# Performance work log

Hardware: AMD Instinct MI355X
Metric: run time of the kernel (lower is better)

The kernel has to match this reference:

```python
import jax, jax.numpy as jnp
import numpy as np

N_NODES = 100000
N_EDGES = 1250000
D = 64
K = 5
EPS = 1e-8


def setup_inputs() -> dict:
    key = jax.random.key(0)
    k1, k2, k3, k4 = jax.random.split(key, 4)
    x = jax.random.normal(k1, (N_NODES, D), dtype=jnp.float32)
    mask = jax.random.normal(k2, (N_NODES, 1), dtype=jnp.float32)
    edge_index = jax.random.randint(k3, (2, N_EDGES), 0, N_NODES, dtype=jnp.int64)
    # orthogonal-ish init for the linear layer (QR of gaussian), gain for tanh = 5/3
    g = jax.random.normal(k4, (D, D), dtype=jnp.float32)
    q, _ = jnp.linalg.qr(g)
    W = (5.0 / 3.0) * q.astype(jnp.float32)
    b = jnp.zeros((D,), dtype=jnp.float32)
    alpha = jnp.float32(0.001)
    return {"x": x, "mask": mask, "edge_index": edge_index, "W": W, "b": b, "alpha": alpha}


def _forward(x, mask, edge_index, W, b, alpha):
    n = x.shape[0]
    # x_fn: Linear + Tanh
    h = jnp.tanh(x @ W.T + b)  # [N, D]
    src = edge_index[0]
    dst = edge_index[1]
    hs = h[src]  # [E, D] gather
    hd = h[dst]  # [E, D] gather
    # torch cosine_similarity with eps clamp on each norm
    ns = jnp.maximum(jnp.sqrt(jnp.sum(hs * hs, axis=-1)), EPS)
    nd = jnp.maximum(jnp.sqrt(jnp.sum(hd * hd, axis=-1)), EPS)
    cos = jnp.sum(hs * hd, axis=-1) / (ns * nd)
    edge_weights = jax.nn.relu(cos)  # [E]

    # gcn_norm with self loops (PyG APPNP default): D^-1/2 (A + I) D^-1/2
    loop = jnp.arange(n, dtype=src.dtype)
    row = jnp.concatenate([src, loop])
    col = jnp.concatenate([dst, loop])
    w = jnp.concatenate([edge_weights, jnp.ones((n,), dtype=edge_weights.dtype)])
    deg = jax.ops.segment_sum(w, col, num_segments=n)
    dis = jnp.where(deg > 0, jax.lax.rsqrt(jnp.maximum(deg, EPS)), 0.0)
    norm_w = dis[row] * w * dis[col]  # [E + N]

    # APPNP: K steps of f = (1-alpha) * A_hat @ f + alpha * f0
    f0 = jax.nn.relu(mask)  # [N, 1]
    f = f0
    for _ in range(K):
        msg = norm_w[:, None] * f[row]  # gather + weight
        agg = jax.ops.segment_sum(msg, col, num_segments=n)  # scatter-add
        f = (1.0 - alpha) * agg + alpha * f0
    return f, edge_weights


def reference(x, mask, edge_index, W, b, alpha):
    return _forward(x, mask, edge_index, W, b, alpha)
```

## Files before the change

### kernel.cpp

```cpp
#include <hip/hip_runtime.h>
#include <hip/hip_fp16.h>
#include <math.h>

#define N_NODES 100000
#define N_EDGES 1250000
#define D 64
#define EPS 1e-8f

#define ZERO_BLOCKS 391
#define GEMM_BLOCKS 1024
#define RANK_BLOCKS 4883

__global__ __launch_bounds__(256) void k_gemm_zero(
    const float* __restrict__ x, const float* __restrict__ W,
    const float* __restrict__ b, __half* __restrict__ hn, int* __restrict__ cnt)
{
    if (blockIdx.x < ZERO_BLOCKS) {
        int i = blockIdx.x * 256 + threadIdx.x;
        if (i < N_NODES) cnt[i] = 0;
        return;
    }
    __shared__ float xrow[4][72];
    const int lane = threadIdx.x & 63;
    const int wid  = threadIdx.x >> 6;

    float Wreg[64];
    const float4* Wv = (const float4*)(W + lane * D);
    #pragma unroll
    for (int q = 0; q < 16; ++q) {
        float4 w4 = Wv[q];
        Wreg[4*q+0] = w4.x; Wreg[4*q+1] = w4.y;
        Wreg[4*q+2] = w4.z; Wreg[4*q+3] = w4.w;
    }
    const float bj = b[lane];
    float* xl = xrow[wid];

    const int wave   = (blockIdx.x - ZERO_BLOCKS) * 4 + wid;
    const int nwaves = GEMM_BLOCKS * 4;

    for (int row = wave; row < N_NODES; row += nwaves) {
        float xv = x[(size_t)row * D + lane];
        xl[lane] = xv;
        float acc = bj;
        #pragma unroll
        for (int q = 0; q < 16; ++q) {
            float4 xk4 = *(const float4*)(xl + 4*q);
            acc = fmaf(xk4.x, Wreg[4*q+0], acc);
            acc = fmaf(xk4.y, Wreg[4*q+1], acc);
            acc = fmaf(xk4.z, Wreg[4*q+2], acc);
            acc = fmaf(xk4.w, Wreg[4*q+3], acc);
        }
        float h = tanhf(acc);
        float s = h * h;
        #pragma unroll
        for (int m = 32; m >= 1; m >>= 1) s += __shfl_xor(s, m, 64);
        float nrm = fmaxf(sqrtf(s), EPS);
        hn[(size_t)row * D + lane] = __float2half_rn(h / nrm);
    }
}

__device__ __forceinline__ float dot8h(float4 a, float4 c)
{
    const __half2* ah = (const __half2*)&a;
    const __half2* ch = (const __half2*)&c;
    float p = 0.0f;
    #pragma unroll
    for (int q = 0; q < 4; ++q) {
        float2 af = __half22float2(ah[q]);
        float2 cf = __half22float2(ch[q]);
        p = fmaf(af.x, cf.x, p);
        p = fmaf(af.y, cf.y, p);
    }
    return p;
}

__global__ __launch_bounds__(256) void k_rank_cos(
    const int* __restrict__ ei, int* __restrict__ cnt, int* __restrict__ rank,
    const __half* __restrict__ hn, float* __restrict__ wout)
{
    const int b = blockIdx.x;
    const int r = b % 3;
    if (r == 0) {
        int e = (b / 3) * 256 + threadIdx.x;
        if (e < N_EDGES) {
            int d = ei[N_EDGES + e];
            rank[e] = atomicAdd(cnt + d, 1);
        }
        return;
    }
    int cb = (b / 3) * 2 + (r - 1);
    int t = cb * 256 + threadIdx.x;
    int g = t >> 3, sub = t & 7;
    if (g >= N_EDGES / 4) return;
    int e0 = g * 4;
    int4 ss = *(const int4*)(ei + e0);
    int4 dd = *(const int4*)(ei + N_EDGES + e0);

    float4 a0 = ((const float4*)(hn + (size_t)ss.x * D))[sub];
    float4 c0 = ((const float4*)(hn + (size_t)dd.x * D))[sub];
    float4 a1 = ((const float4*)(hn + (size_t)ss.y * D))[sub];
    float4 c1 = ((const float4*)(hn + (size_t)dd.y * D))[sub];
    float4 a2 = ((const float4*)(hn + (size_t)ss.z * D))[sub];
    float4 c2 = ((const float4*)(hn + (size_t)dd.z * D))[sub];
    float4 a3 = ((const float4*)(hn + (size_t)ss.w * D))[sub];
    float4 c3 = ((const float4*)(hn + (size_t)dd.w * D))[sub];

    float p0 = dot8h(a0, c0);
    float p1 = dot8h(a1, c1);
    float p2 = dot8h(a2, c2);
    float p3 = dot8h(a3, c3);
    p0 += __shfl_xor(p0, 1, 64);  p1 += __shfl_xor(p1, 1, 64);
    p2 += __shfl_xor(p2, 1, 64);  p3 += __shfl_xor(p3, 1, 64);
    p0 += __shfl_xor(p0, 2, 64);  p1 += __shfl_xor(p1, 2, 64);
    p2 += __shfl_xor(p2, 2, 64);  p3 += __shfl_xor(p3, 2, 64);
    p0 += __shfl_xor(p0, 4, 64);  p1 += __shfl_xor(p1, 4, 64);
    p2 += __shfl_xor(p2, 4, 64);  p3 += __shfl_xor(p3, 4, 64);

    if (sub == 0) {
        *(float4*)(wout + e0) = make_float4(
            fmaxf(p0, 0.0f), fmaxf(p1, 0.0f), fmaxf(p2, 0.0f), fmaxf(p3, 0.0f));
    }
}

__device__ __forceinline__ int wave_iscan(int v, int lane)
{
    int incl = v;
    #pragma unroll
    for (int m = 1; m < 64; m <<= 1) {
        int o = __shfl_up(incl, m, 64);
        if (lane >= m) incl += o;
    }
    return incl;
}

__global__ __launch_bounds__(256) void k_scan1(
    const int* __restrict__ cnt, int* __restrict__ rowptr, int* __restrict__ bsum)
{
    __shared__ int wsum[4];
    int t = threadIdx.x, b = blockIdx.x;
    int i = b * 256 + t;
    int lane = t & 63, wid = t >> 6;
    int v = (i < N_NODES) ? cnt[i] : 0;
    int incl = wave_iscan(v, lane);
    if (lane == 63) wsum[wid] = incl;
    __syncthreads();
    int off = 0;
    #pragma unroll
    for (int k = 0; k < 4; ++k) if (k < wid) off += wsum[k];
    if (i < N_NODES) rowptr[i] = off + incl - v;
    if (t == 255) bsum[b] = off + incl;
}

__global__ __launch_bounds__(512) void k_scan2(
    const int* __restrict__ bsum, int* __restrict__ boff, int nblk)
{
    __shared__ int wsum[8];
    int t = threadIdx.x;
    int lane = t & 63, wid = t >> 6;
    int v = (t < nblk) ? bsum[t] : 0;
    int incl = wave_iscan(v, lane);
    if (lane == 63) wsum[wid] = incl;
    __syncthreads();
    int off = 0;
    #pragma unroll
    for (int k = 0; k < 8; ++k) if (k < wid) off += wsum[k];
    if (t < nblk) boff[t] = off + incl - v;
}

__global__ __launch_bounds__(256) void k_scan3(
    int* __restrict__ rowptr, const int* __restrict__ boff)
{
    int i = blockIdx.x * 256 + threadIdx.x;
    if (i < N_NODES) rowptr[i] += boff[i >> 8];
    if (i == 0) rowptr[N_NODES] = N_EDGES;
}

__global__ __launch_bounds__(256) void k_place(
    const int* __restrict__ ei, const int* __restrict__ rank_pos,
    const int* __restrict__ rowptr, const float* __restrict__ wsrc,
    int2* __restrict__ pairs)
{
    int e = blockIdx.x * 256 + threadIdx.x;
    if (e >= N_EDGES) return;
    int s = ei[e];
    int d = ei[N_EDGES + e];
    int pos = rowptr[d] + rank_pos[e];
    pairs[pos] = make_int2(s, __float_as_int(wsrc[e]));
}

__global__ __launch_bounds__(256) void k_dis_y(
    const int* __restrict__ rowptr, const int2* __restrict__ pairs,
    const float* __restrict__ mask, float* __restrict__ dis,
    float* __restrict__ y)
{
    int t = blockIdx.x * 256 + threadIdx.x;
    int node = t >> 4, l = t & 15;
    if (node >= N_NODES) return;
    int beg = rowptr[node], end = rowptr[node + 1];
    float s = 0.0f;
    for (int j = beg + l; j < end; j += 16)
        s += __int_as_float(pairs[j].y);
    s += __shfl_xor(s, 1, 64);
    s += __shfl_xor(s, 2, 64);
    s += __shfl_xor(s, 4, 64);
    s += __shfl_xor(s, 8, 64);
    if (l == 0) {
        float di = rsqrtf(fmaxf(s + 1.0f, EPS));
        dis[node] = di;
        y[node] = di * fmaxf(mask[node], 0.0f);
    }
}

__global__ __launch_bounds__(256) void k_spmv(
    const int* __restrict__ rowptr, const int2* __restrict__ pairs,
    const float* __restrict__ y_in, const float* __restrict__ dis,
    const float* __restrict__ mask, const float* __restrict__ alpha_p,
    float* __restrict__ y_out, float* __restrict__ f_out)
{
    int t = blockIdx.x * 256 + threadIdx.x;
    int node = t >> 4, l = t & 15;
    if (node >= N_NODES) return;
    int beg = rowptr[node], end = rowptr[node + 1];
    float sum = 0.0f;
    for (int j = beg + l; j < end; j += 16) {
        int2 p = pairs[j];
        sum += __int_as_float(p.y) * y_in[p.x];
    }
    sum += __shfl_xor(sum, 1, 64);
    sum += __shfl_xor(sum, 2, 64);
    sum += __shfl_xor(sum, 4, 64);
    sum += __shfl_xor(sum, 8, 64);
    if (l == 0) {
        float di = dis[node];
        float alpha = alpha_p[0];
        float f0 = fmaxf(mask[node], 0.0f);
        float fn = (1.0f - alpha) * di * (sum + y_in[node]) + alpha * f0;
        f_out[node] = fn;
        y_out[node] = di * fn;
    }
}

extern "C" void kernel_launch(void* const* d_in, const int* in_sizes, int n_in,
                              void* d_out, int out_size, void* d_ws, size_t ws_size,
                              hipStream_t stream)
{
    const float* x     = (const float*)d_in[0];
    const float* mask  = (const float*)d_in[1];
    const int*   ei    = (const int*)  d_in[2];
    const float* W     = (const float*)d_in[3];
    const float* b     = (const float*)d_in[4];
    const float* alpha = (const float*)d_in[5];

    float* out_f = (float*)d_out;
    float* out_w = (float*)d_out + N_NODES;

    float* ws = (float*)d_ws;
    __half* hn     = (__half*)ws;
    int2*  pairs   = (int2*) (ws + 3200000);
    int*   rank    = (int*)  (ws + 5700000);
    int*   cnt     = (int*)  (ws + 6950000);
    int*   rowptr  = (int*)  (ws + 7050000);
    float* dis     =          ws + 7150016;
    float* y_a     =          ws + 7250016;
    float* y_b     =          ws + 7350016;
    float* f_scr   =          ws + 7450016;
    int*   bsum    = (int*)  (ws + 7550016);
    int*   boff    = (int*)  (ws + 7550528);

    const int nodeBlocks = (N_NODES + 255) / 256;
    const int edgeBlocks = (N_EDGES + 255) / 256;
    const int segBlocks  = (int)(((long long)N_NODES * 16 + 255) / 256);

    k_gemm_zero<<<ZERO_BLOCKS + GEMM_BLOCKS, 256, 0, stream>>>(x, W, b, hn, cnt);
    k_rank_cos<<<3 * RANK_BLOCKS, 256, 0, stream>>>(ei, cnt, rank, hn, out_w);
    k_scan1<<<nodeBlocks, 256, 0, stream>>>(cnt, rowptr, bsum);
    k_scan2<<<1, 512, 0, stream>>>(bsum, boff, nodeBlocks);
    k_scan3<<<nodeBlocks, 256, 0, stream>>>(rowptr, boff);
    k_place<<<edgeBlocks, 256, 0, stream>>>(ei, rank, rowptr, out_w, pairs);
    k_dis_y<<<segBlocks, 256, 0, stream>>>(rowptr, pairs, mask, dis, y_a);

    k_spmv<<<segBlocks, 256, 0, stream>>>(rowptr, pairs, y_a, dis, mask, alpha, y_b, f_scr);
    k_spmv<<<segBlocks, 256, 0, stream>>>(rowptr, pairs, y_b, dis, mask, alpha, y_a, f_scr);
    k_spmv<<<segBlocks, 256, 0, stream>>>(rowptr, pairs, y_a, dis, mask, alpha, y_b, f_scr);
    k_spmv<<<segBlocks, 256, 0, stream>>>(rowptr, pairs, y_b, dis, mask, alpha, y_a, f_scr);
    k_spmv<<<segBlocks, 256, 0, stream>>>(rowptr, pairs, y_a, dis, mask, alpha, y_b, out_f);
}
```

Baseline: 247.0 us.

## Fuse degree computation into cosine kernel, fold scan offsets, narrow SpMV lanes

```diff
diff --git a/kernel.cpp b/kernel.cpp
--- a/kernel.cpp
+++ b/kernel.cpp
@@ -10,14 +10,17 @@
 #define ZERO_BLOCKS 391
 #define GEMM_BLOCKS 1024
 #define RANK_BLOCKS 4883
+#define EDGE_BLOCKS 4883
+#define NODE_BLOCKS 391
 
 __global__ __launch_bounds__(256) void k_gemm_zero(
     const float* __restrict__ x, const float* __restrict__ W,
-    const float* __restrict__ b, __half* __restrict__ hn, int* __restrict__ cnt)
+    const float* __restrict__ b, __half* __restrict__ hn,
+    int* __restrict__ cnt, float* __restrict__ deg)
 {
     if (blockIdx.x < ZERO_BLOCKS) {
         int i = blockIdx.x * 256 + threadIdx.x;
-        if (i < N_NODES) cnt[i] = 0;
+        if (i < N_NODES) { cnt[i] = 0; deg[i] = 0.0f; }
         return;
     }
     __shared__ float xrow[4][72];
@@ -76,7 +79,8 @@
 
 __global__ __launch_bounds__(256) void k_rank_cos(
     const int* __restrict__ ei, int* __restrict__ cnt, int* __restrict__ rank,
-    const __half* __restrict__ hn, float* __restrict__ wout)
+    const __half* __restrict__ hn, float* __restrict__ wout,
+    float* __restrict__ deg)
 {
     const int b = blockIdx.x;
     const int r = b % 3;
@@ -117,8 +121,15 @@
     p2 += __shfl_xor(p2, 4, 64);  p3 += __shfl_xor(p3, 4, 64);
 
     if (sub == 0) {
-        *(float4*)(wout + e0) = make_float4(
-            fmaxf(p0, 0.0f), fmaxf(p1, 0.0f), fmaxf(p2, 0.0f), fmaxf(p3, 0.0f));
+        float w0 = fmaxf(p0, 0.0f);
+        float w1 = fmaxf(p1, 0.0f);
+        float w2 = fmaxf(p2, 0.0f);
+        float w3 = fmaxf(p3, 0.0f);
+        *(float4*)(wout + e0) = make_float4(w0, w1, w2, w3);
+        atomicAdd(deg + dd.x, w0);
+        atomicAdd(deg + dd.y, w1);
+        atomicAdd(deg + dd.z, w2);
+        atomicAdd(deg + dd.w, w3);
     }
 }
 
@@ -152,7 +163,8 @@
 }
 
 __global__ __launch_bounds__(512) void k_scan2(
-    const int* __restrict__ bsum, int* __restrict__ boff, int nblk)
+    const int* __restrict__ bsum, int* __restrict__ boff, int nblk,
+    int* __restrict__ rowptr)
 {
     __shared__ int wsum[8];
     int t = threadIdx.x;
@@ -165,71 +177,54 @@
     #pragma unroll
     for (int k = 0; k < 8; ++k) if (k < wid) off += wsum[k];
     if (t < nblk) boff[t] = off + incl - v;
-}
-
-__global__ __launch_bounds__(256) void k_scan3(
-    int* __restrict__ rowptr, const int* __restrict__ boff)
-{
-    int i = blockIdx.x * 256 + threadIdx.x;
-    if (i < N_NODES) rowptr[i] += boff[i >> 8];
-    if (i == 0) rowptr[N_NODES] = N_EDGES;
-}
-
-__global__ __launch_bounds__(256) void k_place(
+    if (t == 0) rowptr[N_NODES] = N_EDGES;
+}
+
+__global__ __launch_bounds__(256) void k_place_dis(
     const int* __restrict__ ei, const int* __restrict__ rank_pos,
-    const int* __restrict__ rowptr, const float* __restrict__ wsrc,
-    int2* __restrict__ pairs)
-{
+    const int* __restrict__ rowptr, const int* __restrict__ boff,
+    const float* __restrict__ wsrc, int2* __restrict__ pairs,
+    const float* __restrict__ deg, const float* __restrict__ mask,
+    float* __restrict__ dis, float* __restrict__ y)
+{
+    if (blockIdx.x >= EDGE_BLOCKS) {
+        int node = (blockIdx.x - EDGE_BLOCKS) * 256 + threadIdx.x;
+        if (node < N_NODES) {
+            float di = rsqrtf(fmaxf(deg[node] + 1.0f, EPS));
+            dis[node] = di;
+            y[node] = di * fmaxf(mask[node], 0.0f);
+        }
+        return;
+    }
     int e = blockIdx.x * 256 + threadIdx.x;
     if (e >= N_EDGES) return;
     int s = ei[e];
     int d = ei[N_EDGES + e];
-    int pos = rowptr[d] + rank_pos[e];
+    int pos = rowptr[d] + boff[d >> 8] + rank_pos[e];
     pairs[pos] = make_int2(s, __float_as_int(wsrc[e]));
 }
 
-__global__ __launch_bounds__(256) void k_dis_y(
-    const int* __restrict__ rowptr, const int2* __restrict__ pairs,
-    const float* __restrict__ mask, float* __restrict__ dis,
-    float* __restrict__ y)
-{
-    int t = blockIdx.x * 256 + threadIdx.x;
-    int node = t >> 4, l = t & 15;
-    if (node >= N_NODES) return;
-    int beg = rowptr[node], end = rowptr[node + 1];
-    float s = 0.0f;
-    for (int j = beg + l; j < end; j += 16)
-        s += __int_as_float(pairs[j].y);
-    s += __shfl_xor(s, 1, 64);
-    s += __shfl_xor(s, 2, 64);
-    s += __shfl_xor(s, 4, 64);
-    s += __shfl_xor(s, 8, 64);
-    if (l == 0) {
-        float di = rsqrtf(fmaxf(s + 1.0f, EPS));
-        dis[node] = di;
-        y[node] = di * fmaxf(mask[node], 0.0f);
-    }
-}
-
 __global__ __launch_bounds__(256) void k_spmv(
-    const int* __restrict__ rowptr, const int2* __restrict__ pairs,
+    const int* __restrict__ rowptr, const int* __restrict__ boff,
+    const int2* __restrict__ pairs,
     const float* __restrict__ y_in, const float* __restrict__ dis,
     const float* __restrict__ mask, const float* __restrict__ alpha_p,
     float* __restrict__ y_out, float* __restrict__ f_out)
 {
     int t = blockIdx.x * 256 + threadIdx.x;
-    int node = t >> 4, l = t & 15;
+    int node = t >> 3, l = t & 7;
     if (node >= N_NODES) return;
-    int beg = rowptr[node], end = rowptr[node + 1];
+    int beg = rowptr[node] + boff[node >> 8];
+    int np1 = node + 1;
+    int end = rowptr[np1] + (np1 < N_NODES ? boff[np1 >> 8] : 0);
     float sum = 0.0f;
-    for (int j = beg + l; j < end; j += 16) {
+    for (int j = beg + l; j < end; j += 8) {
         int2 p = pairs[j];
         sum += __int_as_float(p.y) * y_in[p.x];
     }
     sum += __shfl_xor(sum, 1, 64);
     sum += __shfl_xor(sum, 2, 64);
     sum += __shfl_xor(sum, 4, 64);
-    sum += __shfl_xor(sum, 8, 64);
     if (l == 0) {
         float di = dis[node];
         float alpha = alpha_p[0];
@@ -267,21 +262,20 @@
     int*   bsum    = (int*)  (ws + 7550016);
     int*   boff    = (int*)  (ws + 7550528);
 
-    const int nodeBlocks = (N_NODES + 255) / 256;
-    const int edgeBlocks = (N_EDGES + 255) / 256;
-    const int segBlocks  = (int)(((long long)N_NODES * 16 + 255) / 256);
-
-    k_gemm_zero<<<ZERO_BLOCKS + GEMM_BLOCKS, 256, 0, stream>>>(x, W, b, hn, cnt);
-    k_rank_cos<<<3 * RANK_BLOCKS, 256, 0, stream>>>(ei, cnt, rank, hn, out_w);
-    k_scan1<<<nodeBlocks, 256, 0, stream>>>(cnt, rowptr, bsum);
-    k_scan2<<<1, 512, 0, stream>>>(bsum, boff, nodeBlocks);
-    k_scan3<<<nodeBlocks, 256, 0, stream>>>(rowptr, boff);
-    k_place<<<edgeBlocks, 256, 0, stream>>>(ei, rank, rowptr, out_w, pairs);
-    k_dis_y<<<segBlocks, 256, 0, stream>>>(rowptr, pairs, mask, dis, y_a);
-
-    k_spmv<<<segBlocks, 256, 0, stream>>>(rowptr, pairs, y_a, dis, mask, alpha, y_b, f_scr);
-    k_spmv<<<segBlocks, 256, 0, stream>>>(rowptr, pairs, y_b, dis, mask, alpha, y_a, f_scr);
-    k_spmv<<<segBlocks, 256, 0, stream>>>(rowptr, pairs, y_a, dis, mask, alpha, y_b, f_scr);
-    k_spmv<<<segBlocks, 256, 0, stream>>>(rowptr, pairs, y_b, dis, mask, alpha, y_a, f_scr);
-    k_spmv<<<segBlocks, 256, 0, stream>>>(rowptr, pairs, y_a, dis, mask, alpha, y_b, out_f);
-}
+    float* deg = f_scr;
+
+    const int spmvBlocks = (int)(((long long)N_NODES * 8 + 255) / 256);
+
+    k_gemm_zero<<<ZERO_BLOCKS + GEMM_BLOCKS, 256, 0, stream>>>(x, W, b, hn, cnt, deg);
+    k_rank_cos<<<3 * RANK_BLOCKS, 256, 0, stream>>>(ei, cnt, rank, hn, out_w, deg);
+    k_scan1<<<NODE_BLOCKS, 256, 0, stream>>>(cnt, rowptr, bsum);
+    k_scan2<<<1, 512, 0, stream>>>(bsum, boff, NODE_BLOCKS, rowptr);
+    k_place_dis<<<EDGE_BLOCKS + NODE_BLOCKS, 256, 0, stream>>>(
+        ei, rank, rowptr, boff, out_w, pairs, deg, mask, dis, y_a);
+
+    k_spmv<<<spmvBlocks, 256, 0, stream>>>(rowptr, boff, pairs, y_a, dis, mask, alpha, y_b, f_scr);
+    k_spmv<<<spmvBlocks, 256, 0, stream>>>(rowptr, boff, pairs, y_b, dis, mask, alpha, y_a, f_scr);
+    k_spmv<<<spmvBlocks, 256, 0, stream>>>(rowptr, boff, pairs, y_a, dis, mask, alpha, y_b, f_scr);
+    k_spmv<<<spmvBlocks, 256, 0, stream>>>(rowptr, boff, pairs, y_b, dis, mask, alpha, y_a, f_scr);
+    k_spmv<<<spmvBlocks, 256, 0, stream>>>(rowptr, boff, pairs, y_a, dis, mask, alpha, y_b, out_f);
+}
```

Result: slower. 301.7 us (+22.1%).
